# Optimization experiments

Measured on AMD Instinct MI355X. Metric: run time of the kernel, lower is better.

Reference implementation:

```python
import jax, jax.numpy as jnp
import numpy as np


def _dwconv3(x, w):
    # x: (b, c, L), w: (c, 1, 3) depthwise, padding=1
    return jax.lax.conv_general_dilated(
        x, w, window_strides=(1,), padding=((1, 1),),
        dimension_numbers=('NCH', 'OIH', 'NCH'),
        feature_group_count=x.shape[1])


def _l2norm(x, eps=1e-12):
    # matches torch F.normalize(dim=-1)
    n = jnp.sqrt(jnp.sum(x * x, axis=-1, keepdims=True))
    return x / jnp.maximum(n, eps)


def setup_inputs() -> dict:
    key = jax.random.key(0)
    ks = jax.random.split(key, 7)
    dim, heads, b, L = 64, 4, 4, 131072
    s = 0.02
    return dict(
        x=jax.random.normal(ks[0], (b, dim, L, 1), jnp.float32),
        w_kv=jax.random.normal(ks[1], (2 * dim, dim, 1), jnp.float32) * s,
        w_kv_dw=jax.random.normal(ks[2], (2 * dim, 1, 3), jnp.float32) * s,
        w_q=jax.random.normal(ks[3], (dim, dim, 1), jnp.float32) * s,
        w_q_dw=jax.random.normal(ks[4], (dim, 1, 3), jnp.float32) * s,
        w_proj=jax.random.normal(ks[5], (dim, dim, 1), jnp.float32) * s,
        temperature=jnp.ones((heads, 1, 1), jnp.float32),
    )


def reference(x, w_kv, w_kv_dw, w_q, w_q_dw, w_proj, temperature):
    xs = x[..., 0]  # (b, c, L)
    # kv branch: 1x1 conv then depthwise k=3 conv
    kv = _dwconv3(jnp.einsum('oc,bcl->bol', w_kv[:, :, 0], xs), w_kv_dw)
    k, v = jnp.split(kv, 2, axis=1)  # each (b, c, L)
    # q branch
    q = _dwconv3(jnp.einsum('oc,bcl->bol', w_q[:, :, 0], xs), w_q_dw)
    q = _l2norm(q)
    k = _l2norm(k)
    # channel attention: (b, c, c); temperature (H,1,1) broadcasts over batch (b == num_heads)
    attn = jnp.einsum('bcl,bdl->bcd', q, k) * temperature
    attn = jax.nn.softmax(attn, axis=-1)
    out = jnp.einsum('bcd,bdl->bcl', attn, v)
    out = jnp.einsum('oc,bcl->bol', w_proj[:, :, 0], out)
    return out[..., None]  # (b, c, L, 1)
```

## Files before the change

kernel.cpp:

```cpp
#include <hip/hip_runtime.h>

#define LLEN 131072
#define CDIM 64
#define NB 4
#define TP 62
#define NCH_A 5
#define BLKA 423
#define NCH_C 5
#define BLKC 423
#define XSP 65
#define QHP 72

typedef _Float16 half8 __attribute__((ext_vector_type(8)));
typedef float f32x4 __attribute__((ext_vector_type(4)));
#define MFMA16 __builtin_amdgcn_mfma_f32_16x16x32_f16

__device__ __forceinline__ float dpp_shr1(float v) {
  return __int_as_float(__builtin_amdgcn_update_dpp(
      0, __float_as_int(v), 0x111, 0xF, 0xF, true));
}
__device__ __forceinline__ float dpp_shl1(float v) {
  return __int_as_float(__builtin_amdgcn_update_dpp(
      0, __float_as_int(v), 0x101, 0xF, 0xF, true));
}
template <int PAT>
__device__ __forceinline__ float swz(float v) {
  return __int_as_float(__builtin_amdgcn_ds_swizzle(__float_as_int(v), PAT));
}
#define SWZ_BC15 0x1F0
#define SWZ_BC0  0x010

__device__ __forceinline__ void conv3(f32x4 a[4], const float* dwt, int c) {
  f32x4 o[4];
#pragma unroll
  for (int n = 0; n < 4; ++n) {
#pragma unroll
    for (int r = 0; r < 4; ++r) {
      const float cur = a[n][r];
      float lf = dpp_shr1(cur);
      const float lb = (n > 0) ? swz<SWZ_BC15>(a[n - 1][r]) : 0.f;
      lf = (c == 0) ? lb : lf;
      float rt = dpp_shl1(cur);
      const float rb = (n < 3) ? swz<SWZ_BC0>(a[n + 1][r]) : 0.f;
      rt = (c == 15) ? rb : rt;
      o[n][r] = dwt[0 * 4 + r] * lf + dwt[1 * 4 + r] * cur + dwt[2 * 4 + r] * rt;
    }
  }
#pragma unroll
  for (int n = 0; n < 4; ++n) a[n] = o[n];
}

__device__ __forceinline__ void stage_x(const float* __restrict__ xb,
                                        float* xs, int wv, int lane, int w0) {
  const int p = w0 - 1 + lane;
  const int pc = min(max(p, 0), LLEN - 1);
  const float* g0 = xb + pc;
#pragma unroll
  for (int k = 0; k < 16; ++k) {
    const int r = wv * 16 + k;
    __builtin_amdgcn_global_load_lds(
        (const __attribute__((address_space(1))) void*)(g0 + (size_t)r * LLEN),
        (__attribute__((address_space(3))) void*)(xs + r * XSP), 4, 0, 0);
  }
}

__global__ void prep_kernel(const float* __restrict__ w_q,
                            const float* __restrict__ w_kv,
                            _Float16* __restrict__ wqA, _Float16* __restrict__ wkA,
                            _Float16* __restrict__ wvA) {
  const int t = blockIdx.x * 256 + threadIdx.x;
  const int j = t & 7;
  const int row = t >> 3;
  const int lane = row & 63;
  const int frag = row >> 6;
  const int m = frag >> 1, ks = frag & 1;
  const int ch = m * 16 + (lane & 15);
  const int ci = ks * 32 + ((lane >> 4) & 3) * 8 + j;
  wqA[t] = (_Float16)w_q[ch * 64 + ci];
  wkA[t] = (_Float16)w_kv[ch * 64 + ci];
  wvA[t] = (_Float16)w_kv[(64 + ch) * 64 + ci];
}

__global__ __launch_bounds__(256) void qk_gram_kernel(
    const float* __restrict__ x, const _Float16* __restrict__ wqA,
    const _Float16* __restrict__ wkA, const float* __restrict__ w_q_dw,
    const float* __restrict__ w_kv_dw, float* __restrict__ G,
    float* __restrict__ nq, float* __restrict__ nk) {
  __shared__ __attribute__((aligned(16))) float xs[64 * XSP];
  __shared__ __attribute__((aligned(16))) _Float16 qh[64 * QHP];
  __shared__ __attribute__((aligned(16))) _Float16 kh[64 * QHP];

  const int tid  = threadIdx.x;
  const int lane = tid & 63;
  const int wv   = __builtin_amdgcn_readfirstlane(tid >> 6);
  const int g    = lane >> 4;
  const int c    = lane & 15;
  const int b    = blockIdx.y;

  const float* xb = x + (size_t)b * CDIM * LLEN;

  half8 aQ[2], aK[2];
#pragma unroll
  for (int ks = 0; ks < 2; ++ks) {
    aQ[ks] = *(const half8*)(wqA + ((wv * 2 + ks) * 64 + lane) * 8);
    aK[ks] = *(const half8*)(wkA + ((wv * 2 + ks) * 64 + lane) * 8);
  }
  float dwq[12], dwk[12];
#pragma unroll
  for (int r = 0; r < 4; ++r) {
    const int ch = wv * 16 + g * 4 + r;
#pragma unroll
    for (int t = 0; t < 3; ++t) {
      dwq[t * 4 + r] = w_q_dw[ch * 3 + t];
      dwk[t * 4 + r] = w_kv_dw[ch * 3 + t];
    }
  }

  f32x4 gacc[4];
#pragma unroll
  for (int m = 0; m < 4; ++m)
#pragma unroll
    for (int r = 0; r < 4; ++r) gacc[m][r] = 0.f;
  float nrmq[4] = {0.f, 0.f, 0.f, 0.f}, nrmk[4] = {0.f, 0.f, 0.f, 0.f};

  stage_x(xb, xs, wv, lane, blockIdx.x * NCH_A * TP);
  __syncthreads();

  for (int ck = 0; ck < NCH_A; ++ck) {
    const int w0 = (blockIdx.x * NCH_A + ck) * TP;

    f32x4 qacc[4], kacc[4];
#pragma unroll
    for (int n = 0; n < 4; ++n)
#pragma unroll
      for (int r = 0; r < 4; ++r) { qacc[n][r] = 0.f; kacc[n][r] = 0.f; }

#pragma unroll
    for (int ks = 0; ks < 2; ++ks) {
      half8 bf[4];
#pragma unroll
      for (int n = 0; n < 4; ++n) {
        const float* xcol = xs + (ks * 32 + g * 8) * XSP + n * 16 + c;
#pragma unroll
        for (int j = 0; j < 8; ++j) bf[n][j] = (_Float16)xcol[j * XSP];
      }
#pragma unroll
      for (int n = 0; n < 4; ++n) {
        qacc[n] = MFMA16(aQ[ks], bf[n], qacc[n], 0, 0, 0);
        kacc[n] = MFMA16(aK[ks], bf[n], kacc[n], 0, 0, 0);
      }
    }

#pragma unroll
    for (int n = 0; n < 4; ++n) {
      const int P = w0 - 1 + n * 16 + c;
      const bool pv = (P >= 0) && (P < LLEN);
#pragma unroll
      for (int r = 0; r < 4; ++r) {
        qacc[n][r] = pv ? qacc[n][r] : 0.f;
        kacc[n][r] = pv ? kacc[n][r] : 0.f;
      }
    }
    conv3(qacc, dwq, c);
    conv3(kacc, dwk, c);

    __syncthreads();

#pragma unroll
    for (int n = 0; n < 4; ++n) {
      const int pos = n * 16 + c;
      const bool ok = (pos >= 1) && (pos <= 62) && (w0 - 1 + pos < LLEN);
#pragma unroll
      for (int r = 0; r < 4; ++r) {
        const _Float16 hq = ok ? (_Float16)qacc[n][r] : (_Float16)0.f;
        const _Float16 hk = ok ? (_Float16)kacc[n][r] : (_Float16)0.f;
        const float fq = (float)hq, fk = (float)hk;
        nrmq[r] = fmaf(fq, fq, nrmq[r]);
        nrmk[r] = fmaf(fk, fk, nrmk[r]);
        qh[(wv * 16 + g * 4 + r) * QHP + pos] = hq;
        kh[(wv * 16 + g * 4 + r) * QHP + pos] = hk;
      }
    }

    if (ck + 1 < NCH_A)
      stage_x(xb, xs, wv, lane, (blockIdx.x * NCH_A + ck + 1) * TP);

    __syncthreads();

    {
      const _Float16* kcol = kh + (wv * 16 + c) * QHP + g * 8;
      const half8 bK0 = *(const half8*)(kcol);
      const half8 bK1 = *(const half8*)(kcol + 32);
#pragma unroll
      for (int m = 0; m < 4; ++m) {
        const _Float16* qrow = qh + (m * 16 + c) * QHP + g * 8;
        const half8 a0 = *(const half8*)(qrow);
        const half8 a1 = *(const half8*)(qrow + 32);
        gacc[m] = MFMA16(a0, bK0, gacc[m], 0, 0, 0);
        gacc[m] = MFMA16(a1, bK1, gacc[m], 0, 0, 0);
      }
    }
    __syncthreads();
  }

  float* Gb = G + b * 4096;
#pragma unroll
  for (int m = 0; m < 4; ++m)
#pragma unroll
    for (int r = 0; r < 4; ++r)
      atomicAdd(&Gb[(m * 16 + g * 4 + r) * 64 + wv * 16 + c], gacc[m][r]);

#pragma unroll
  for (int r = 0; r < 4; ++r) {
    nrmq[r] += __shfl_xor(nrmq[r], 1);  nrmk[r] += __shfl_xor(nrmk[r], 1);
    nrmq[r] += __shfl_xor(nrmq[r], 2);  nrmk[r] += __shfl_xor(nrmk[r], 2);
    nrmq[r] += __shfl_xor(nrmq[r], 4);  nrmk[r] += __shfl_xor(nrmk[r], 4);
    nrmq[r] += __shfl_xor(nrmq[r], 8);  nrmk[r] += __shfl_xor(nrmk[r], 8);
  }
  if (c == 0) {
#pragma unroll
    for (int r = 0; r < 4; ++r) {
      atomicAdd(&nq[b * 64 + wv * 16 + g * 4 + r], nrmq[r]);
      atomicAdd(&nk[b * 64 + wv * 16 + g * 4 + r], nrmk[r]);
    }
  }
}

__global__ void attn_proj_kernel(const float* __restrict__ G,
                                 const float* __restrict__ nq,
                                 const float* __restrict__ nk,
                                 const float* __restrict__ w_proj,
                                 const float* __restrict__ temperature,
                                 _Float16* __restrict__ Mh) {
  __shared__ float attn_s[64][65];
  __shared__ float Ms[64][65];
  __shared__ float invq_s[64];
  __shared__ float invk_s[64];
  const int b = blockIdx.x;
  const int tid = threadIdx.x;
  if (tid < 64)       invq_s[tid]      = 1.f / fmaxf(sqrtf(nq[b * 64 + tid]), 1e-12f);
  else if (tid < 128) invk_s[tid - 64] = 1.f / fmaxf(sqrtf(nk[b * 64 + tid - 64]), 1e-12f);
  __syncthreads();
  const float temp = temperature[b];
  if (tid < 64) {
    const int cq = tid;
    const float* Gr = G + b * 4096 + cq * 64;
    const float iq = invq_s[cq] * temp;
    float z[64];
    float m = -1e30f;
#pragma unroll
    for (int d = 0; d < 64; ++d) { z[d] = Gr[d] * iq * invk_s[d]; m = fmaxf(m, z[d]); }
    float s = 0.f;
#pragma unroll
    for (int d = 0; d < 64; ++d) { z[d] = expf(z[d] - m); s += z[d]; }
    const float inv = 1.f / s;
#pragma unroll
    for (int d = 0; d < 64; ++d) attn_s[cq][d] = z[d] * inv;
  }
  __syncthreads();
  const int o = tid & 63;
  const int dg = tid >> 6;
  for (int d = dg * 16; d < dg * 16 + 16; ++d) {
    float s = 0.f;
#pragma unroll
    for (int cc = 0; cc < 64; ++cc) s = fmaf(w_proj[o * 64 + cc], attn_s[cc][d], s);
    Ms[o][d] = s;
  }
  __syncthreads();
  for (int e = tid; e < 512; e += 256) {
    const int lane_ = e & 63, frag = e >> 6;
    const int m = frag >> 1, ks = frag & 1;
    const int o_ = m * 16 + (lane_ & 15);
    const int d0 = ks * 32 + ((lane_ >> 4) & 3) * 8;
    _Float16* dst = Mh + b * 4096 + e * 8;
#pragma unroll
    for (int j = 0; j < 8; ++j) dst[j] = (_Float16)Ms[o_][d0 + j];
  }
}

__global__ __launch_bounds__(256) void out_kernel(
    const float* __restrict__ x, const _Float16* __restrict__ wvA,
    const float* __restrict__ w_kv_dw, const _Float16* __restrict__ Mh,
    float* __restrict__ out) {
  __shared__ __attribute__((aligned(16))) float xs[64 * XSP];
  __shared__ __attribute__((aligned(16))) _Float16 vh[64 * QHP];

  const int tid  = threadIdx.x;
  const int lane = tid & 63;
  const int wv   = __builtin_amdgcn_readfirstlane(tid >> 6);
  const int g    = lane >> 4;
  const int c    = lane & 15;
  const int b    = blockIdx.y;

  const float* xb = x + (size_t)b * CDIM * LLEN;
  float* ob = out + (size_t)b * CDIM * LLEN;

  half8 aV[2], aM[2];
#pragma unroll
  for (int ks = 0; ks < 2; ++ks) {
    aV[ks] = *(const half8*)(wvA + ((wv * 2 + ks) * 64 + lane) * 8);
    aM[ks] = *(const half8*)(Mh + b * 4096 + ((wv * 2 + ks) * 64 + lane) * 8);
  }
  float dwv[12];
#pragma unroll
  for (int r = 0; r < 4; ++r) {
    const int ch = wv * 16 + g * 4 + r;
#pragma unroll
    for (int t = 0; t < 3; ++t) dwv[t * 4 + r] = w_kv_dw[(64 + ch) * 3 + t];
  }

  stage_x(xb, xs, wv, lane, blockIdx.x * NCH_C * TP);
  __syncthreads();

  for (int ck = 0; ck < NCH_C; ++ck) {
    const int w0 = (blockIdx.x * NCH_C + ck) * TP;

    f32x4 vacc[4];
#pragma unroll
    for (int n = 0; n < 4; ++n)
#pragma unroll
      for (int r = 0; r < 4; ++r) vacc[n][r] = 0.f;

#pragma unroll
    for (int ks = 0; ks < 2; ++ks) {
      half8 bf[4];
#pragma unroll
      for (int n = 0; n < 4; ++n) {
        const float* xcol = xs + (ks * 32 + g * 8) * XSP + n * 16 + c;
#pragma unroll
        for (int j = 0; j < 8; ++j) bf[n][j] = (_Float16)xcol[j * XSP];
      }
#pragma unroll
      for (int n = 0; n < 4; ++n)
        vacc[n] = MFMA16(aV[ks], bf[n], vacc[n], 0, 0, 0);
    }

#pragma unroll
    for (int n = 0; n < 4; ++n) {
      const int P = w0 - 1 + n * 16 + c;
      const bool pv = (P >= 0) && (P < LLEN);
#pragma unroll
      for (int r = 0; r < 4; ++r) vacc[n][r] = pv ? vacc[n][r] : 0.f;
    }
    conv3(vacc, dwv, c);

    __syncthreads();

#pragma unroll
    for (int n = 0; n < 4; ++n) {
      const int pos = n * 16 + c;
      const bool ok = (pos >= 1) && (pos <= 62) && (w0 - 1 + pos < LLEN);
#pragma unroll
      for (int r = 0; r < 4; ++r) {
        const _Float16 hv = ok ? (_Float16)vacc[n][r] : (_Float16)0.f;
        vh[pos * QHP + wv * 16 + g * 4 + r] = hv;
      }
    }

    if (ck + 1 < NCH_C)
      stage_x(xb, xs, wv, lane, (blockIdx.x * NCH_C + ck + 1) * TP);

    __syncthreads();

    f32x4 oacc[4];
#pragma unroll
    for (int n = 0; n < 4; ++n)
#pragma unroll
      for (int r = 0; r < 4; ++r) oacc[n][r] = 0.f;
#pragma unroll
    for (int n = 0; n < 4; ++n) {
      const _Float16* vrow = vh + (n * 16 + c) * QHP + g * 8;
      const half8 b0 = *(const half8*)(vrow);
      const half8 b1 = *(const half8*)(vrow + 32);
      oacc[n] = MFMA16(aM[0], b0, oacc[n], 0, 0, 0);
      oacc[n] = MFMA16(aM[1], b1, oacc[n], 0, 0, 0);
    }
#pragma unroll
    for (int n = 0; n < 4; ++n) {
      const int pos = n * 16 + c;
      const int P = w0 - 1 + pos;
      if (pos >= 1 && pos <= 62 && P < LLEN) {
#pragma unroll
        for (int r = 0; r < 4; ++r)
          ob[(size_t)(wv * 16 + g * 4 + r) * LLEN + P] = oacc[n][r];
      }
    }
    __syncthreads();
  }
}

extern "C" void kernel_launch(void* const* d_in, const int* in_sizes, int n_in,
                              void* d_out, int out_size, void* d_ws, size_t ws_size,
                              hipStream_t stream) {
  (void)in_sizes; (void)n_in; (void)out_size; (void)ws_size;
  const float* x           = (const float*)d_in[0];
  const float* w_kv        = (const float*)d_in[1];
  const float* w_kv_dw     = (const float*)d_in[2];
  const float* w_q         = (const float*)d_in[3];
  const float* w_q_dw      = (const float*)d_in[4];
  const float* w_proj      = (const float*)d_in[5];
  const float* temperature = (const float*)d_in[6];
  float* out = (float*)d_out;

  float* G   = (float*)d_ws;
  float* nqp = G + 16384;
  float* nkp = nqp + 256;
  _Float16* Mh  = (_Float16*)(nkp + 256);
  _Float16* wqA = Mh + NB * 4096;
  _Float16* wkA = wqA + 4096;
  _Float16* wvA = wkA + 4096;

  (void)hipMemsetAsync(G, 0, (size_t)(16384 + 512) * sizeof(float), stream);
  prep_kernel<<<dim3(16), dim3(256), 0, stream>>>(w_q, w_kv, wqA, wkA, wvA);
  qk_gram_kernel<<<dim3(BLKA, NB), dim3(256), 0, stream>>>(
      x, wqA, wkA, w_q_dw, w_kv_dw, G, nqp, nkp);
  attn_proj_kernel<<<dim3(NB), dim3(256), 0, stream>>>(
      G, nqp, nkp, w_proj, temperature, Mh);
  out_kernel<<<dim3(BLKC, NB), dim3(256), 0, stream>>>(
      x, wvA, w_kv_dw, Mh, out);
}
```

Measured before the change: 412.6 us.

## Pre-convert staged x tile to fp16 fragments and issue next-chunk loads earlier

Each chunk's fp32 x tile is now converted cooperatively, once, into fp16 MFMA B-fragment layout in a shared buffer, with boundary masking applied at that point. This replaces per-wave strided scalar LDS reads and converts, and removes the mask on the accumulators. Because xs is freed sooner, the async global-to-LDS prefetch of the next chunk is issued right after conversion, giving it more compute to overlap with. It also widens the xs row pitch to 66 for float2 reads, packs the v-store into half4 writes, reuses the k/v buffer for the fragments, and adds occupancy hints to launch_bounds. The cost is an extra barrier per chunk and possible register pressure from the occupancy targets.

```diff
diff --git a/kernel.cpp b/kernel.cpp
--- a/kernel.cpp
+++ b/kernel.cpp
@@ -8,10 +8,11 @@
 #define BLKA 423
 #define NCH_C 5
 #define BLKC 423
-#define XSP 65
+#define XSP 66
 #define QHP 72
 
 typedef _Float16 half8 __attribute__((ext_vector_type(8)));
+typedef _Float16 half4 __attribute__((ext_vector_type(4)));
 typedef float f32x4 __attribute__((ext_vector_type(4)));
 #define MFMA16 __builtin_amdgcn_mfma_f32_16x16x32_f16
 
@@ -62,6 +63,28 @@
         (const __attribute__((address_space(1))) void*)(g0 + (size_t)r * LLEN),
         (__attribute__((address_space(3))) void*)(xs + r * XSP), 4, 0, 0);
   }
+}
+
+__device__ __forceinline__ void convert_xf(const float* __restrict__ xs,
+                                           _Float16* __restrict__ xf,
+                                           int tid, int w0) {
+  const int f   = tid >> 5;
+  const int l0  = (tid & 31) * 2;
+  const int ks  = f >> 2, n = f & 3;
+  const int ci0 = ks * 32 + (l0 >> 4) * 8;
+  const int pos = n * 16 + (l0 & 15);
+  const int P0  = w0 - 1 + pos;
+  const bool v0 = (P0 >= 0) && (P0 < LLEN);
+  const bool v1 = (P0 + 1 >= 0) && (P0 + 1 < LLEN);
+  half8 h0, h1;
+#pragma unroll
+  for (int j = 0; j < 8; ++j) {
+    const float2 s = *(const float2*)&xs[(ci0 + j) * XSP + pos];
+    h0[j] = (_Float16)(v0 ? s.x : 0.f);
+    h1[j] = (_Float16)(v1 ? s.y : 0.f);
+  }
+  *(half8*)(xf + (f * 64 + l0) * 8) = h0;
+  *(half8*)(xf + (f * 64 + l0 + 1) * 8) = h1;
 }
 
 __global__ void prep_kernel(const float* __restrict__ w_q,
@@ -81,14 +104,14 @@
   wvA[t] = (_Float16)w_kv[(64 + ch) * 64 + ci];
 }
 
-__global__ __launch_bounds__(256) void qk_gram_kernel(
+__global__ __launch_bounds__(256, 4) void qk_gram_kernel(
     const float* __restrict__ x, const _Float16* __restrict__ wqA,
     const _Float16* __restrict__ wkA, const float* __restrict__ w_q_dw,
     const float* __restrict__ w_kv_dw, float* __restrict__ G,
     float* __restrict__ nq, float* __restrict__ nk) {
   __shared__ __attribute__((aligned(16))) float xs[64 * XSP];
   __shared__ __attribute__((aligned(16))) _Float16 qh[64 * QHP];
-  __shared__ __attribute__((aligned(16))) _Float16 kh[64 * QHP];
+  __shared__ __attribute__((aligned(16))) _Float16 ku[64 * QHP];
 
   const int tid  = threadIdx.x;
   const int lane = tid & 63;
@@ -129,41 +152,28 @@
   for (int ck = 0; ck < NCH_A; ++ck) {
     const int w0 = (blockIdx.x * NCH_A + ck) * TP;
 
+    convert_xf(xs, ku, tid, w0);
+    __syncthreads();
+
+    if (ck + 1 < NCH_A)
+      stage_x(xb, xs, wv, lane, (blockIdx.x * NCH_A + ck + 1) * TP);
+
     f32x4 qacc[4], kacc[4];
 #pragma unroll
     for (int n = 0; n < 4; ++n)
 #pragma unroll
       for (int r = 0; r < 4; ++r) { qacc[n][r] = 0.f; kacc[n][r] = 0.f; }
-
 #pragma unroll
     for (int ks = 0; ks < 2; ++ks) {
-      half8 bf[4];
 #pragma unroll
       for (int n = 0; n < 4; ++n) {
-        const float* xcol = xs + (ks * 32 + g * 8) * XSP + n * 16 + c;
-#pragma unroll
-        for (int j = 0; j < 8; ++j) bf[n][j] = (_Float16)xcol[j * XSP];
-      }
-#pragma unroll
-      for (int n = 0; n < 4; ++n) {
-        qacc[n] = MFMA16(aQ[ks], bf[n], qacc[n], 0, 0, 0);
-        kacc[n] = MFMA16(aK[ks], bf[n], kacc[n], 0, 0, 0);
-      }
-    }
-
-#pragma unroll
-    for (int n = 0; n < 4; ++n) {
-      const int P = w0 - 1 + n * 16 + c;
-      const bool pv = (P >= 0) && (P < LLEN);
-#pragma unroll
-      for (int r = 0; r < 4; ++r) {
-        qacc[n][r] = pv ? qacc[n][r] : 0.f;
-        kacc[n][r] = pv ? kacc[n][r] : 0.f;
+        const half8 bf = *(const half8*)(ku + ((ks * 4 + n) * 64 + lane) * 8);
+        qacc[n] = MFMA16(aQ[ks], bf, qacc[n], 0, 0, 0);
+        kacc[n] = MFMA16(aK[ks], bf, kacc[n], 0, 0, 0);
       }
     }
     conv3(qacc, dwq, c);
     conv3(kacc, dwk, c);
-
     __syncthreads();
 
 #pragma unroll
@@ -178,17 +188,13 @@
         nrmq[r] = fmaf(fq, fq, nrmq[r]);
         nrmk[r] = fmaf(fk, fk, nrmk[r]);
         qh[(wv * 16 + g * 4 + r) * QHP + pos] = hq;
-        kh[(wv * 16 + g * 4 + r) * QHP + pos] = hk;
+        ku[(wv * 16 + g * 4 + r) * QHP + pos] = hk;
       }
     }
-
-    if (ck + 1 < NCH_A)
-      stage_x(xb, xs, wv, lane, (blockIdx.x * NCH_A + ck + 1) * TP);
-
     __syncthreads();
 
     {
-      const _Float16* kcol = kh + (wv * 16 + c) * QHP + g * 8;
+      const _Float16* kcol = ku + (wv * 16 + c) * QHP + g * 8;
       const half8 bK0 = *(const half8*)(kcol);
       const half8 bK1 = *(const half8*)(kcol + 32);
 #pragma unroll
@@ -278,12 +284,12 @@
   }
 }
 
-__global__ __launch_bounds__(256) void out_kernel(
+__global__ __launch_bounds__(256, 5) void out_kernel(
     const float* __restrict__ x, const _Float16* __restrict__ wvA,
     const float* __restrict__ w_kv_dw, const _Float16* __restrict__ Mh,
     float* __restrict__ out) {
   __shared__ __attribute__((aligned(16))) float xs[64 * XSP];
-  __shared__ __attribute__((aligned(16))) _Float16 vh[64 * QHP];
+  __shared__ __attribute__((aligned(16))) _Float16 vu[64 * QHP];
 
   const int tid  = threadIdx.x;
   const int lane = tid & 63;
@@ -315,51 +321,38 @@
   for (int ck = 0; ck < NCH_C; ++ck) {
     const int w0 = (blockIdx.x * NCH_C + ck) * TP;
 
+    convert_xf(xs, vu, tid, w0);
+    __syncthreads();
+
+    if (ck + 1 < NCH_C)
+      stage_x(xb, xs, wv, lane, (blockIdx.x * NCH_C + ck + 1) * TP);
+
     f32x4 vacc[4];
 #pragma unroll
     for (int n = 0; n < 4; ++n)
 #pragma unroll
       for (int r = 0; r < 4; ++r) vacc[n][r] = 0.f;
-
 #pragma unroll
     for (int ks = 0; ks < 2; ++ks) {
-      half8 bf[4];
 #pragma unroll
       for (int n = 0; n < 4; ++n) {
-        const float* xcol = xs + (ks * 32 + g * 8) * XSP + n * 16 + c;
-#pragma unroll
-        for (int j = 0; j < 8; ++j) bf[n][j] = (_Float16)xcol[j * XSP];
+        const half8 bf = *(const half8*)(vu + ((ks * 4 + n) * 64 + lane) * 8);
+        vacc[n] = MFMA16(aV[ks], bf, vacc[n], 0, 0, 0);
       }
-#pragma unroll
-      for (int n = 0; n < 4; ++n)
-        vacc[n] = MFMA16(aV[ks], bf[n], vacc[n], 0, 0, 0);
-    }
-
-#pragma unroll
-    for (int n = 0; n < 4; ++n) {
-      const int P = w0 - 1 + n * 16 + c;
-      const bool pv = (P >= 0) && (P < LLEN);
-#pragma unroll
-      for (int r = 0; r < 4; ++r) vacc[n][r] = pv ? vacc[n][r] : 0.f;
     }
     conv3(vacc, dwv, c);
-
     __syncthreads();
 
 #pragma unroll
     for (int n = 0; n < 4; ++n) {
       const int pos = n * 16 + c;
       const bool ok = (pos >= 1) && (pos <= 62) && (w0 - 1 + pos < LLEN);
-#pragma unroll
-      for (int r = 0; r < 4; ++r) {
-        const _Float16 hv = ok ? (_Float16)vacc[n][r] : (_Float16)0.f;
-        vh[pos * QHP + wv * 16 + g * 4 + r] = hv;
-      }
-    }
-
-    if (ck + 1 < NCH_C)
-      stage_x(xb, xs, wv, lane, (blockIdx.x * NCH_C + ck + 1) * TP);
-
+      half4 hv;
+#pragma unroll
+      for (int r = 0; r < 4; ++r)
+        hv[r] = ok ? (_Float16)vacc[n][r] : (_Float16)0.f;
+      *(half4*)(vu + pos * QHP + wv * 16 + g * 4) = hv;
+    }
     __syncthreads();
 
     f32x4 oacc[4];
@@ -369,7 +362,7 @@
       for (int r = 0; r < 4; ++r) oacc[n][r] = 0.f;
 #pragma unroll
     for (int n = 0; n < 4; ++n) {
-      const _Float16* vrow = vh + (n * 16 + c) * QHP + g * 8;
+      const _Float16* vrow = vu + (n * 16 + c) * QHP + g * 8;
       const half8 b0 = *(const half8*)(vrow);
       const half8 b1 = *(const half8*)(vrow + 32);
       oacc[n] = MFMA16(aM[0], b0, oacc[n], 0, 0, 0);
```

Measured after the change: 500.5 us. +21.3%, slower.
